# Kernel tuning notes

Hardware: AMD Instinct MI355X
Metric: run time of the kernel (lower is better)

The kernel has to match this reference:

```python
import jax, jax.numpy as jnp
import numpy as np

H = 512          # hidden_dim
T = 20           # output_seq_len
EPS = 1e-5


def _ln(x, g, b):
    m = jnp.mean(x, axis=-1, keepdims=True)
    v = jnp.mean((x - m) ** 2, axis=-1, keepdims=True)
    return (x - m) * jax.lax.rsqrt(v + EPS) * g + b


def setup_inputs() -> dict:
    key = jax.random.key(0)
    ks = jax.random.split(key, 20)
    N, LD, PD = 65536, 128, 32
    s = 0.02
    return {
        "z_q": jax.random.normal(ks[0], (N, LD), jnp.float32),
        "f_prior": jax.random.normal(ks[1], (N, PD), jnp.float32),
        # init_mlp: Linear(160 -> 1024) -> LN -> GELU -> Linear(1024 -> 512) -> Tanh
        "W1": jax.random.normal(ks[2], (LD + PD, 2 * H), jnp.float32) * s,
        "b1": jnp.zeros((2 * H,), jnp.float32),
        "g1": jnp.ones((2 * H,), jnp.float32),
        "be1": jnp.zeros((2 * H,), jnp.float32),
        "W2": jax.random.normal(ks[3], (2 * H, H), jnp.float32) * s,
        "b2": jnp.zeros((H,), jnp.float32),
        # start token (output_dim = 1)
        "start_token": jax.random.normal(ks[4], (1,), jnp.float32) * 0.1,
        # GRU, input_size=1, hidden_size=H, gates stacked [r, z, n] (torch layout)
        "W_ih": jax.random.normal(ks[5], (3 * H, 1), jnp.float32) * s,
        "W_hh": jax.random.normal(ks[6], (3 * H, H), jnp.float32) * s,
        "b_ih": jnp.zeros((3 * H,), jnp.float32),
        "b_hh": jnp.zeros((3 * H,), jnp.float32),
        # output_mlp: Linear(H -> H//2) -> LN -> GELU -> Linear(H//2 -> 1)
        "Wo1": jax.random.normal(ks[7], (H, H // 2), jnp.float32) * s,
        "bo1": jnp.zeros((H // 2,), jnp.float32),
        "go": jnp.ones((H // 2,), jnp.float32),
        "beo": jnp.zeros((H // 2,), jnp.float32),
        "Wo2": jax.random.normal(ks[8], (H // 2, 1), jnp.float32) * s,
        "bo2": jnp.zeros((1,), jnp.float32),
    }


def reference(z_q, f_prior, W1, b1, g1, be1, W2, b2, start_token,
              W_ih, W_hh, b_ih, b_hh, Wo1, bo1, go, beo, Wo2, bo2):
    N = z_q.shape[0]
    # init_mlp -> h_0 (dropout is identity at eval)
    combined = jnp.concatenate([z_q, f_prior], axis=1)          # (N, LD+PD)
    h = jnp.tanh(jax.nn.gelu(_ln(combined @ W1 + b1, g1, be1), approximate=False) @ W2 + b2)  # (N, H)

    x0 = jnp.broadcast_to(start_token[None, :], (N, 1))          # (N, 1)

    def step(carry, _):
        h, x = carry
        gi = x @ W_ih.T + b_ih                                   # (N, 3H)
        gh = h @ W_hh.T + b_hh                                   # (N, 3H)
        r = jax.nn.sigmoid(gi[:, :H] + gh[:, :H])
        z = jax.nn.sigmoid(gi[:, H:2 * H] + gh[:, H:2 * H])
        n = jnp.tanh(gi[:, 2 * H:] + r * gh[:, 2 * H:])
        h_new = (1.0 - z) * n + z * h
        y = jax.nn.gelu(_ln(h_new @ Wo1 + bo1, go, beo), approximate=False) @ Wo2 + bo2  # (N, 1)
        return (h_new, y), y

    _, ys = jax.lax.scan(step, (h, x0), None, length=T)          # (T, N, 1)
    preds = jnp.transpose(ys[..., 0], (1, 0))                    # (N, T), output_dim==1 squeeze
    return preds
```

## Files before the change

kernel.cpp:

```cpp
#include <hip/hip_runtime.h>
#include <math.h>


typedef _Float16 f16;
typedef _Float16 f16x4 __attribute__((ext_vector_type(4)));
typedef _Float16 f16x8 __attribute__((ext_vector_type(8)));
typedef float f32x4 __attribute__((ext_vector_type(4)));

#define TSTEPS 20

__device__ __forceinline__ float sigm(float v) { return 1.0f / (1.0f + __expf(-v)); }
__device__ __forceinline__ float tanh_s(float v) {
  float e = __expf(-2.0f * fabsf(v));
  float r = (1.0f - e) / (1.0f + e);
  return copysignf(r, v);
}
__device__ __forceinline__ float gelu_e(float v) {
  return 0.5f * v * (1.0f + erff(v * 0.70710678118654752f));
}
__device__ __forceinline__ void st4(float* d, float4 v) {
  d[0] = v.x; d[1] = v.y; d[2] = v.z; d[3] = v.w;
}

__device__ __forceinline__ int fa(int m, int k) {
  return (((k >> 5) * 4 + (m >> 4)) << 10) + (((m & 15) + ((k >> 3) & 3) * 16) << 4) + ((k & 7) * 2);
}

__global__ void cvt_weights(const float* __restrict__ W1, const float* __restrict__ W2,
                            const float* __restrict__ Whh, const float* __restrict__ Wo1,
                            const float* __restrict__ bih, const float* __restrict__ bhh,
                            f16* __restrict__ w1t, f16* __restrict__ w2t,
                            f16* __restrict__ whh, f16* __restrict__ wo1t,
                            float* __restrict__ bcr, float* __restrict__ bcz) {
  int i = blockIdx.x * 256 + threadIdx.x;
  if (i < 163840) { int n = i / 160; int k = i - n * 160; w1t[i] = (f16)W1[k * 1024 + n]; return; }
  i -= 163840;
  if (i < 524288) { int n = i >> 10; int k = i & 1023; w2t[i] = (f16)W2[k * 512 + n]; return; }
  i -= 524288;
  if (i < 786432) { whh[i] = (f16)Whh[i]; return; }
  i -= 786432;
  if (i < 131072) { int o = i >> 9; int k = i & 511; wo1t[i] = (f16)Wo1[k * 256 + o]; return; }
  i -= 131072;
  if (i < 512) { bcr[i] = bih[i] + bhh[i]; return; }
  i -= 512;
  if (i < 512) { bcz[i] = bih[512 + i] + bhh[512 + i]; return; }
}

__global__ __launch_bounds__(512, 2)
void gru_main(
    const float* __restrict__ zq, const float* __restrict__ fpr,
    const float* __restrict__ b1, const float* __restrict__ g1, const float* __restrict__ be1,
    const float* __restrict__ b2, const float* __restrict__ stok,
    const float* __restrict__ Wih, const float* __restrict__ bih, const float* __restrict__ bhh,
    const float* __restrict__ bo1, const float* __restrict__ go, const float* __restrict__ beo,
    const float* __restrict__ Wo2, const float* __restrict__ bo2,
    const f16* __restrict__ w1t, const f16* __restrict__ w2t,
    const f16* __restrict__ whh, const f16* __restrict__ wo1t,
    const float* __restrict__ bcr, const float* __restrict__ bcz,
    float* __restrict__ out) {
  __shared__ __align__(16) unsigned char sm[131072];
  __shared__ float sm_s[256], sm_ss[256], sm_yp[256];
  __shared__ float sm_x[64];

  const int tid = threadIdx.x;
  const int w = tid >> 6;
  const int lane = tid & 63;
  const int l16 = lane & 15;
  const int l4 = lane >> 4;
  const int R0 = blockIdx.x * 64;

  const float bo2v = bo2[0];
  if (tid < 64) sm_x[tid] = stok[0];

  #pragma unroll 1
  for (int p = 0; p < 4; ++p) {
    #pragma unroll 1
    for (int jh = 0; jh < 2; ++jh) {
      const int jq0 = w * 128 + p * 32 + jh * 16;
      f32x4 acc[4];
      #pragma unroll
      for (int mt = 0; mt < 4; ++mt) acc[mt] = (f32x4){0.f, 0.f, 0.f, 0.f};
      #pragma unroll
      for (int kf = 0; kf < 5; ++kf) {
        const int k0 = kf * 32 + l4 * 8;
        f16x8 B[4];
        #pragma unroll
        for (int mt = 0; mt < 4; ++mt) {
          const int gm = R0 + mt * 16 + l16;
          const float* src = (kf < 4) ? (zq + gm * 128 + k0) : (fpr + gm * 32 + (k0 - 128));
          float4 v0 = *(const float4*)src;
          float4 v1 = *(const float4*)(src + 4);
          f16x8 b;
          b[0] = (f16)v0.x; b[1] = (f16)v0.y; b[2] = (f16)v0.z; b[3] = (f16)v0.w;
          b[4] = (f16)v1.x; b[5] = (f16)v1.y; b[6] = (f16)v1.z; b[7] = (f16)v1.w;
          B[mt] = b;
        }
        const f16x8 A = *(const f16x8*)(w1t + (jq0 + l16) * 160 + k0);
        #pragma unroll
        for (int mt = 0; mt < 4; ++mt)
          acc[mt] = __builtin_amdgcn_mfma_f32_16x16x32_f16(A, B[mt], acc[mt], 0, 0, 0);
      }
      const int jq = jq0 + l4 * 4;
      float bb[4]; st4(bb, *(const float4*)(b1 + jq));
      #pragma unroll
      for (int mt = 0; mt < 4; ++mt) {
        f16x4 v;
        #pragma unroll
        for (int r = 0; r < 4; ++r) v[r] = (f16)(acc[mt][r] + bb[r]);
        *(f16x4*)(sm + fa(mt * 16 + l16, jq)) = v;
      }
    }
  }
  __syncthreads();
  {
    const int mt = w & 3, half = w >> 2;
    const int row = mt * 16 + l16;
    float s = 0.f, ss = 0.f;
    #pragma unroll 4
    for (int it = 0; it < 16; ++it) {
      const int kb = half * 16 + it;
      f16x8 v = *(const f16x8*)(sm + (kb * 4 + mt) * 1024 + lane * 16);
      #pragma unroll
      for (int i = 0; i < 8; ++i) { float f = (float)v[i]; s += f; ss += f * f; }
    }
    s += __shfl_xor(s, 16); ss += __shfl_xor(ss, 16);
    s += __shfl_xor(s, 32); ss += __shfl_xor(ss, 32);
    if (l4 == 0) { sm_s[row * 2 + half] = s; sm_ss[row * 2 + half] = ss; }
    __syncthreads();
    const float mean = (sm_s[row * 2] + sm_s[row * 2 + 1]) * (1.f / 1024.f);
    const float q2 = (sm_ss[row * 2] + sm_ss[row * 2 + 1]) * (1.f / 1024.f);
    const float rstd = rsqrtf(q2 - mean * mean + 1e-5f);
    #pragma unroll 2
    for (int it = 0; it < 16; ++it) {
      const int kb = half * 16 + it;
      const int off = (kb * 4 + mt) * 1024 + lane * 16;
      const int c = kb * 32 + l4 * 8;
      f16x8 v = *(const f16x8*)(sm + off);
      float4 ga = *(const float4*)(g1 + c);
      float4 gb = *(const float4*)(g1 + c + 4);
      float4 ba = *(const float4*)(be1 + c);
      float4 bb = *(const float4*)(be1 + c + 4);
      float gs[8] = {ga.x, ga.y, ga.z, ga.w, gb.x, gb.y, gb.z, gb.w};
      float bs[8] = {ba.x, ba.y, ba.z, ba.w, bb.x, bb.y, bb.z, bb.w};
      f16x8 o;
      #pragma unroll
      for (int i = 0; i < 8; ++i)
        o[i] = (f16)gelu_e(((float)v[i] - mean) * rstd * gs[i] + bs[i]);
      *(f16x8*)(sm + off) = o;
    }
  }
  __syncthreads();
  f16x4 hold[4][4];
  #pragma unroll 1
  for (int pp = 0; pp < 4; ++pp) {
    const int jq0 = w * 64 + pp * 16;
    f32x4 acc[4];
    #pragma unroll
    for (int mt = 0; mt < 4; ++mt) acc[mt] = (f32x4){0.f, 0.f, 0.f, 0.f};
    #pragma unroll 2
    for (int kf = 0; kf < 32; ++kf) {
      f16x8 B[4];
      #pragma unroll
      for (int mt = 0; mt < 4; ++mt)
        B[mt] = *(const f16x8*)(sm + (kf * 4 + mt) * 1024 + lane * 16);
      const f16x8 A = *(const f16x8*)(w2t + (jq0 + l16) * 1024 + kf * 32 + l4 * 8);
      #pragma unroll
      for (int mt = 0; mt < 4; ++mt)
        acc[mt] = __builtin_amdgcn_mfma_f32_16x16x32_f16(A, B[mt], acc[mt], 0, 0, 0);
    }
    const int jq = jq0 + l4 * 4;
    float bb[4]; st4(bb, *(const float4*)(b2 + jq));
    #pragma unroll
    for (int mt = 0; mt < 4; ++mt) {
      f16x4 v;
      #pragma unroll
      for (int r = 0; r < 4; ++r) v[r] = (f16)tanh_s(acc[mt][r] + bb[r]);
      hold[pp][mt] = v;
    }
  }
  __syncthreads();
  #pragma unroll
  for (int pp = 0; pp < 4; ++pp) {
    const int jq = w * 64 + pp * 16 + l4 * 4;
    #pragma unroll
    for (int mt = 0; mt < 4; ++mt)
      *(f16x4*)(sm + fa(mt * 16 + l16, jq)) = hold[pp][mt];
  }
  __syncthreads();

  #pragma unroll 1
  for (int t = 0; t < TSTEPS; ++t) {
    const int cur = (t & 1) << 16;
    const int nxt = cur ^ 65536;
    #pragma unroll 1
    for (int p = 0; p < 2; ++p) {
      f32x4 acc[4][3][2];
      #pragma unroll
      for (int mt = 0; mt < 4; ++mt)
        #pragma unroll
        for (int g = 0; g < 3; ++g)
          #pragma unroll
          for (int jh = 0; jh < 2; ++jh) acc[mt][g][jh] = (f32x4){0.f, 0.f, 0.f, 0.f};
      #pragma unroll 2
      for (int kf = 0; kf < 16; ++kf) {
        f16x8 B[4];
        #pragma unroll
        for (int mt = 0; mt < 4; ++mt)
          B[mt] = *(const f16x8*)(sm + cur + (kf * 4 + mt) * 1024 + lane * 16);
        #pragma unroll
        for (int g = 0; g < 3; ++g)
          #pragma unroll
          for (int jh = 0; jh < 2; ++jh) {
            const f16x8 A = *(const f16x8*)(whh + (g * 512 + w * 64 + p * 32 + jh * 16 + l16) * 512 + kf * 32 + l4 * 8);
            #pragma unroll
            for (int mt = 0; mt < 4; ++mt)
              acc[mt][g][jh] = __builtin_amdgcn_mfma_f32_16x16x32_f16(A, B[mt], acc[mt][g][jh], 0, 0, 0);
          }
      }
      if (p == 0) __syncthreads();
      #pragma unroll
      for (int jh = 0; jh < 2; ++jh) {
        const int jq = w * 64 + p * 32 + jh * 16 + l4 * 4;
        float wr[4], wz[4], wn[4], cr[4], cz[4], bn[4], cn[4];
        st4(wr, *(const float4*)(Wih + jq));
        st4(wz, *(const float4*)(Wih + 512 + jq));
        st4(wn, *(const float4*)(Wih + 1024 + jq));
        st4(cr, *(const float4*)(bcr + jq));
        st4(cz, *(const float4*)(bcz + jq));
        st4(bn, *(const float4*)(bih + 1024 + jq));
        st4(cn, *(const float4*)(bhh + 1024 + jq));
        #pragma unroll
        for (int mt = 0; mt < 4; ++mt) {
          const int m = mt * 16 + l16;
          const float x = sm_x[m];
          const int hoff = fa(m, jq);
          const f16x4 ho = *(const f16x4*)(sm + cur + hoff);
          f16x4 hn;
          #pragma unroll
          for (int r = 0; r < 4; ++r) {
            const float gr = sigm(x * wr[r] + cr[r] + acc[mt][0][jh][r]);
            const float gz = sigm(x * wz[r] + cz[r] + acc[mt][1][jh][r]);
            const float gn = tanh_s(x * wn[r] + bn[r] + gr * (acc[mt][2][jh][r] + cn[r]));
            hn[r] = (f16)((1.f - gz) * gn + gz * (float)ho[r]);
          }
          *(f16x4*)(sm + nxt + hoff) = hn;
        }
      }
    }
    __syncthreads();
    {
      const int mg = w >> 2, jg = w & 3;
      f32x4 a2[2][4];
      #pragma unroll
      for (int mi = 0; mi < 2; ++mi)
        #pragma unroll
        for (int jt2 = 0; jt2 < 4; ++jt2) a2[mi][jt2] = (f32x4){0.f, 0.f, 0.f, 0.f};
      #pragma unroll 2
      for (int kf = 0; kf < 16; ++kf) {
        f16x8 B[2];
        #pragma unroll
        for (int mi = 0; mi < 2; ++mi)
          B[mi] = *(const f16x8*)(sm + nxt + (kf * 4 + mg * 2 + mi) * 1024 + lane * 16);
        #pragma unroll
        for (int jt2 = 0; jt2 < 4; ++jt2) {
          const f16x8 A = *(const f16x8*)(wo1t + (jg * 64 + jt2 * 16 + l16) * 512 + kf * 32 + l4 * 8);
          #pragma unroll
          for (int mi = 0; mi < 2; ++mi)
            a2[mi][jt2] = __builtin_amdgcn_mfma_f32_16x16x32_f16(A, B[mi], a2[mi][jt2], 0, 0, 0);
        }
      }
      float vv[2][4][4];
      float bo1v[4][4];
      #pragma unroll
      for (int jt2 = 0; jt2 < 4; ++jt2)
        st4(bo1v[jt2], *(const float4*)(bo1 + jg * 64 + jt2 * 16 + l4 * 4));
      #pragma unroll
      for (int mi = 0; mi < 2; ++mi) {
        float s = 0.f, ss = 0.f;
        #pragma unroll
        for (int jt2 = 0; jt2 < 4; ++jt2)
          #pragma unroll
          for (int r = 0; r < 4; ++r) {
            const float v = a2[mi][jt2][r] + bo1v[jt2][r];
            vv[mi][jt2][r] = v; s += v; ss += v * v;
          }
        s += __shfl_xor(s, 16); ss += __shfl_xor(ss, 16);
        s += __shfl_xor(s, 32); ss += __shfl_xor(ss, 32);
        if (l4 == 0) {
          const int m = (mg * 2 + mi) * 16 + l16;
          sm_s[m * 4 + jg] = s;
          sm_ss[m * 4 + jg] = ss;
        }
      }
      __syncthreads();
      float gov[4][4], bev[4][4], wv[4][4];
      #pragma unroll
      for (int jt2 = 0; jt2 < 4; ++jt2) {
        const int jb = jg * 64 + jt2 * 16 + l4 * 4;
        st4(gov[jt2], *(const float4*)(go + jb));
        st4(bev[jt2], *(const float4*)(beo + jb));
        st4(wv[jt2], *(const float4*)(Wo2 + jb));
      }
      #pragma unroll
      for (int mi = 0; mi < 2; ++mi) {
        const int m = (mg * 2 + mi) * 16 + l16;
        float4 ps = *(const float4*)(sm_s + m * 4);
        float4 pq = *(const float4*)(sm_ss + m * 4);
        const float mean = (ps.x + ps.y + ps.z + ps.w) * (1.f / 256.f);
        const float q2 = (pq.x + pq.y + pq.z + pq.w) * (1.f / 256.f);
        const float rstd = rsqrtf(q2 - mean * mean + 1e-5f);
        float y = 0.f;
        #pragma unroll
        for (int jt2 = 0; jt2 < 4; ++jt2)
          #pragma unroll
          for (int r = 0; r < 4; ++r)
            y += gelu_e((vv[mi][jt2][r] - mean) * rstd * gov[jt2][r] + bev[jt2][r]) * wv[jt2][r];
        y += __shfl_xor(y, 16);
        y += __shfl_xor(y, 32);
        if (l4 == 0) sm_yp[m * 4 + jg] = y;
      }
      __syncthreads();
      if (tid < 64) {
        float4 ps = *(const float4*)(sm_yp + tid * 4);
        const float y = bo2v + ps.x + ps.y + ps.z + ps.w;
        sm_x[tid] = y;
        out[(R0 + tid) * 20 + t] = y;
      }
    }
  }
}

extern "C" void kernel_launch(void* const* d_in, const int* in_sizes, int n_in,
                              void* d_out, int out_size, void* d_ws, size_t ws_size,
                              hipStream_t stream) {
  const float* zq   = (const float*)d_in[0];
  const float* fpr  = (const float*)d_in[1];
  const float* W1   = (const float*)d_in[2];
  const float* b1   = (const float*)d_in[3];
  const float* g1   = (const float*)d_in[4];
  const float* be1  = (const float*)d_in[5];
  const float* W2   = (const float*)d_in[6];
  const float* b2   = (const float*)d_in[7];
  const float* stok = (const float*)d_in[8];
  const float* Wih  = (const float*)d_in[9];
  const float* Whh  = (const float*)d_in[10];
  const float* bih  = (const float*)d_in[11];
  const float* bhh  = (const float*)d_in[12];
  const float* Wo1  = (const float*)d_in[13];
  const float* bo1  = (const float*)d_in[14];
  const float* go   = (const float*)d_in[15];
  const float* beo  = (const float*)d_in[16];
  const float* Wo2  = (const float*)d_in[17];
  const float* bo2  = (const float*)d_in[18];

  char* ws = (char*)d_ws;
  f16* w1t   = (f16*)(ws + 0);
  f16* w2t   = (f16*)(ws + 327680);
  f16* whh   = (f16*)(ws + 1376256);
  f16* wo1t  = (f16*)(ws + 2949120);
  float* bcr = (float*)(ws + 3211264);
  float* bcz = (float*)(ws + 3213312);

  cvt_weights<<<6276, 256, 0, stream>>>(W1, W2, Whh, Wo1, bih, bhh,
                                        w1t, w2t, whh, wo1t, bcr, bcz);

  const int N = in_sizes[0] / 128;
  gru_main<<<N / 64, 512, 0, stream>>>(zq, fpr, b1, g1, be1, b2, stok, Wih, bih, bhh,
                                       bo1, go, beo, Wo2, bo2, w1t, w2t, whh, wo1t,
                                       bcr, bcz, (float*)d_out);
}
```

Before: 5.997 ms.

## Warp-specialize GRU step and output MLP, pipelining output of previous step

Waves 0-3 now compute the recurrent GRU matmul and gate blend for step t, while waves 4-7 compute the output MLP for step t-1 from the same hidden-state buffer. Each output wave owns a 16-row tile with the full 256-wide reduction, so the layer-norm statistics no longer need cross-wave shared-memory reductions and extra barriers. Gate weights, combined biases and output LN constants are staged in LDS as f16. The trade-off is that the GRU matmul runs on only half the waves, lengthening the critical path. The f16 constants slightly reduce precision.

```diff
diff --git a/kernel.cpp b/kernel.cpp
--- a/kernel.cpp
+++ b/kernel.cpp
@@ -26,12 +26,59 @@
   return (((k >> 5) * 4 + (m >> 4)) << 10) + (((m & 15) + ((k >> 3) & 3) * 16) << 4) + ((k & 7) * 2);
 }
 
+#define G1_MFMA(ACC, JT)                                                        \
+  {                                                                             \
+    _Pragma("unroll 2")                                                         \
+    for (int kf = 0; kf < 16; ++kf) {                                           \
+      f16x8 Bf[4];                                                              \
+      _Pragma("unroll")                                                         \
+      for (int mt = 0; mt < 4; ++mt)                                            \
+        Bf[mt] = *(const f16x8*)(sm + cur + ((kf * 4 + mt) << 10) + lane * 16); \
+      _Pragma("unroll")                                                         \
+      for (int g = 0; g < 3; ++g) {                                             \
+        const f16x8 Af = *(const f16x8*)(whh + (g * 512 + (JT) + l16) * 512 + kf * 32 + l4 * 8); \
+        _Pragma("unroll")                                                       \
+        for (int mt = 0; mt < 4; ++mt)                                          \
+          ACC[mt][g] = __builtin_amdgcn_mfma_f32_16x16x32_f16(Af, Bf[mt], ACC[mt][g], 0, 0, 0); \
+      }                                                                         \
+    }                                                                           \
+  }
+
+#define G1_BLEND(ACC, JT)                                                       \
+  {                                                                             \
+    const int jq = (JT) + l4 * 4;                                               \
+    const f16x4 wrh = *(const f16x4*)(sm_c7 + jq);                              \
+    const f16x4 wzh = *(const f16x4*)(sm_c7 + 512 + jq);                        \
+    const f16x4 wnh = *(const f16x4*)(sm_c7 + 1024 + jq);                       \
+    const f16x4 crh = *(const f16x4*)(sm_c7 + 1536 + jq);                       \
+    const f16x4 czh = *(const f16x4*)(sm_c7 + 2048 + jq);                       \
+    const f16x4 bnh = *(const f16x4*)(sm_c7 + 2560 + jq);                       \
+    const f16x4 cnh = *(const f16x4*)(sm_c7 + 3072 + jq);                       \
+    _Pragma("unroll")                                                           \
+    for (int mt = 0; mt < 4; ++mt) {                                            \
+      const int m = mt * 16 + l16;                                              \
+      const float x = sm_x[m];                                                  \
+      const int hoff = fa(m, jq);                                               \
+      const f16x4 ho = *(const f16x4*)(sm + cur + hoff);                        \
+      f16x4 hn;                                                                 \
+      _Pragma("unroll")                                                         \
+      for (int r = 0; r < 4; ++r) {                                             \
+        const float gr = sigm(x * (float)wrh[r] + (float)crh[r] + ACC[mt][0][r]); \
+        const float gz = sigm(x * (float)wzh[r] + (float)czh[r] + ACC[mt][1][r]); \
+        const float gn = tanh_s(x * (float)wnh[r] + (float)bnh[r] + gr * (ACC[mt][2][r] + (float)cnh[r])); \
+        hn[r] = (f16)((1.f - gz) * gn + gz * (float)ho[r]);                     \
+      }                                                                         \
+      *(f16x4*)(sm + nxt + hoff) = hn;                                          \
+    }                                                                           \
+  }
+
 __global__ void cvt_weights(const float* __restrict__ W1, const float* __restrict__ W2,
                             const float* __restrict__ Whh, const float* __restrict__ Wo1,
-                            const float* __restrict__ bih, const float* __restrict__ bhh,
+                            const float* __restrict__ Wih, const float* __restrict__ bih,
+                            const float* __restrict__ bhh,
                             f16* __restrict__ w1t, f16* __restrict__ w2t,
                             f16* __restrict__ whh, f16* __restrict__ wo1t,
-                            float* __restrict__ bcr, float* __restrict__ bcz) {
+                            f16* __restrict__ c7) {
   int i = blockIdx.x * 256 + threadIdx.x;
   if (i < 163840) { int n = i / 160; int k = i - n * 160; w1t[i] = (f16)W1[k * 1024 + n]; return; }
   i -= 163840;
@@ -41,9 +88,18 @@
   i -= 786432;
   if (i < 131072) { int o = i >> 9; int k = i & 511; wo1t[i] = (f16)Wo1[k * 256 + o]; return; }
   i -= 131072;
-  if (i < 512) { bcr[i] = bih[i] + bhh[i]; return; }
-  i -= 512;
-  if (i < 512) { bcz[i] = bih[512 + i] + bhh[512 + i]; return; }
+  if (i < 3584) {
+    const int which = i >> 9, j = i & 511;
+    float v;
+    if (which == 0) v = Wih[j];
+    else if (which == 1) v = Wih[512 + j];
+    else if (which == 2) v = Wih[1024 + j];
+    else if (which == 3) v = bih[j] + bhh[j];
+    else if (which == 4) v = bih[512 + j] + bhh[512 + j];
+    else if (which == 5) v = bih[1024 + j];
+    else v = bhh[1024 + j];
+    c7[i] = (f16)v;
+  }
 }
 
 __global__ __launch_bounds__(512, 2)
@@ -51,16 +107,17 @@
     const float* __restrict__ zq, const float* __restrict__ fpr,
     const float* __restrict__ b1, const float* __restrict__ g1, const float* __restrict__ be1,
     const float* __restrict__ b2, const float* __restrict__ stok,
-    const float* __restrict__ Wih, const float* __restrict__ bih, const float* __restrict__ bhh,
     const float* __restrict__ bo1, const float* __restrict__ go, const float* __restrict__ beo,
     const float* __restrict__ Wo2, const float* __restrict__ bo2,
     const f16* __restrict__ w1t, const f16* __restrict__ w2t,
     const f16* __restrict__ whh, const f16* __restrict__ wo1t,
-    const float* __restrict__ bcr, const float* __restrict__ bcz,
+    const f16* __restrict__ c7,
     float* __restrict__ out) {
   __shared__ __align__(16) unsigned char sm[131072];
-  __shared__ float sm_s[256], sm_ss[256], sm_yp[256];
+  __shared__ float sm_s[256], sm_ss[256];
   __shared__ float sm_x[64];
+  __shared__ __align__(8) f16 sm_c7[3584];
+  __shared__ __align__(8) f16 sm_aux[1024];
 
   const int tid = threadIdx.x;
   const int w = tid >> 6;
@@ -71,6 +128,12 @@
 
   const float bo2v = bo2[0];
   if (tid < 64) sm_x[tid] = stok[0];
+  for (int i = tid; i < 1792; i += 512)
+    ((unsigned*)sm_c7)[i] = ((const unsigned*)c7)[i];
+  for (int i = tid; i < 1024; i += 512) {
+    const float v = (i < 256) ? bo1[i] : (i < 512) ? go[i - 256] : (i < 768) ? beo[i - 512] : Wo2[i - 768];
+    sm_aux[i] = (f16)v;
+  }
 
   #pragma unroll 1
   for (int p = 0; p < 4; ++p) {
@@ -144,14 +207,14 @@
       float bs[8] = {ba.x, ba.y, ba.z, ba.w, bb.x, bb.y, bb.z, bb.w};
       f16x8 o;
       #pragma unroll
-      for (int i = 0; i < 8; ++i)
-        o[i] = (f16)gelu_e(((float)v[i] - mean) * rstd * gs[i] + bs[i]);
+      for (int j = 0; j < 8; ++j)
+        o[j] = (f16)gelu_e(((float)v[j] - mean) * rstd * gs[j] + bs[j]);
       *(f16x8*)(sm + off) = o;
     }
   }
   __syncthreads();
   f16x4 hold[4][4];
-  #pragma unroll 1
+  #pragma unroll
   for (int pp = 0; pp < 4; ++pp) {
     const int jq0 = w * 64 + pp * 16;
     f32x4 acc[4];
@@ -162,7 +225,7 @@
       f16x8 B[4];
       #pragma unroll
       for (int mt = 0; mt < 4; ++mt)
-        B[mt] = *(const f16x8*)(sm + (kf * 4 + mt) * 1024 + lane * 16);
+        B[mt] = *(const f16x8*)(sm + ((kf * 4 + mt) << 10) + lane * 16);
       const f16x8 A = *(const f16x8*)(w2t + (jq0 + l16) * 1024 + kf * 32 + l4 * 8);
       #pragma unroll
       for (int mt = 0; mt < 4; ++mt)
@@ -189,144 +252,85 @@
   __syncthreads();
 
   #pragma unroll 1
-  for (int t = 0; t < TSTEPS; ++t) {
+  for (int t = 0; t <= TSTEPS; ++t) {
     const int cur = (t & 1) << 16;
     const int nxt = cur ^ 65536;
-    #pragma unroll 1
-    for (int p = 0; p < 2; ++p) {
-      f32x4 acc[4][3][2];
-      #pragma unroll
-      for (int mt = 0; mt < 4; ++mt)
-        #pragma unroll
-        for (int g = 0; g < 3; ++g)
-          #pragma unroll
-          for (int jh = 0; jh < 2; ++jh) acc[mt][g][jh] = (f32x4){0.f, 0.f, 0.f, 0.f};
-      #pragma unroll 2
-      for (int kf = 0; kf < 16; ++kf) {
-        f16x8 B[4];
+    const int jt0 = w * 128;
+    f32x4 acc0[4][3];
+    if (w < 4) {
+      if (t < TSTEPS) {
         #pragma unroll
         for (int mt = 0; mt < 4; ++mt)
-          B[mt] = *(const f16x8*)(sm + cur + (kf * 4 + mt) * 1024 + lane * 16);
-        #pragma unroll
-        for (int g = 0; g < 3; ++g)
-          #pragma unroll
-          for (int jh = 0; jh < 2; ++jh) {
-            const f16x8 A = *(const f16x8*)(whh + (g * 512 + w * 64 + p * 32 + jh * 16 + l16) * 512 + kf * 32 + l4 * 8);
-            #pragma unroll
-            for (int mt = 0; mt < 4; ++mt)
-              acc[mt][g][jh] = __builtin_amdgcn_mfma_f32_16x16x32_f16(A, B[mt], acc[mt][g][jh], 0, 0, 0);
+          #pragma unroll
+          for (int g = 0; g < 3; ++g) acc0[mt][g] = (f32x4){0.f, 0.f, 0.f, 0.f};
+        G1_MFMA(acc0, jt0)
+      }
+    } else {
+      if (t >= 1) {
+        const int b = w - 4;
+        f32x4 a2[16];
+        #pragma unroll
+        for (int jt = 0; jt < 16; ++jt) a2[jt] = (f32x4){0.f, 0.f, 0.f, 0.f};
+        #pragma unroll 1
+        for (int kf = 0; kf < 16; ++kf) {
+          const f16x8 B = *(const f16x8*)(sm + cur + ((kf * 4 + b) << 10) + lane * 16);
+          #pragma unroll
+          for (int jt = 0; jt < 16; ++jt) {
+            const f16x8 A = *(const f16x8*)(wo1t + (jt * 16 + l16) * 512 + kf * 32 + l4 * 8);
+            a2[jt] = __builtin_amdgcn_mfma_f32_16x16x32_f16(A, B, a2[jt], 0, 0, 0);
           }
-      }
-      if (p == 0) __syncthreads();
-      #pragma unroll
-      for (int jh = 0; jh < 2; ++jh) {
-        const int jq = w * 64 + p * 32 + jh * 16 + l4 * 4;
-        float wr[4], wz[4], wn[4], cr[4], cz[4], bn[4], cn[4];
-        st4(wr, *(const float4*)(Wih + jq));
-        st4(wz, *(const float4*)(Wih + 512 + jq));
-        st4(wn, *(const float4*)(Wih + 1024 + jq));
-        st4(cr, *(const float4*)(bcr + jq));
-        st4(cz, *(const float4*)(bcz + jq));
-        st4(bn, *(const float4*)(bih + 1024 + jq));
-        st4(cn, *(const float4*)(bhh + 1024 + jq));
-        #pragma unroll
-        for (int mt = 0; mt < 4; ++mt) {
-          const int m = mt * 16 + l16;
-          const float x = sm_x[m];
-          const int hoff = fa(m, jq);
-          const f16x4 ho = *(const f16x4*)(sm + cur + hoff);
-          f16x4 hn;
+        }
+        float s = 0.f, ss = 0.f;
+        #pragma unroll
+        for (int jt = 0; jt < 16; ++jt) {
+          const f16x4 bb = *(const f16x4*)(sm_aux + jt * 16 + l4 * 4);
           #pragma unroll
           for (int r = 0; r < 4; ++r) {
-            const float gr = sigm(x * wr[r] + cr[r] + acc[mt][0][jh][r]);
-            const float gz = sigm(x * wz[r] + cz[r] + acc[mt][1][jh][r]);
-            const float gn = tanh_s(x * wn[r] + bn[r] + gr * (acc[mt][2][jh][r] + cn[r]));
-            hn[r] = (f16)((1.f - gz) * gn + gz * (float)ho[r]);
+            const float v = a2[jt][r] + (float)bb[r];
+            a2[jt][r] = v; s += v; ss += v * v;
           }
-          *(f16x4*)(sm + nxt + hoff) = hn;
-        }
-      }
-    }
-    __syncthreads();
-    {
-      const int mg = w >> 2, jg = w & 3;
-      f32x4 a2[2][4];
-      #pragma unroll
-      for (int mi = 0; mi < 2; ++mi)
-        #pragma unroll
-        for (int jt2 = 0; jt2 < 4; ++jt2) a2[mi][jt2] = (f32x4){0.f, 0.f, 0.f, 0.f};
-      #pragma unroll 2
-      for (int kf = 0; kf < 16; ++kf) {
-        f16x8 B[2];
-        #pragma unroll
-        for (int mi = 0; mi < 2; ++mi)
-          B[mi] = *(const f16x8*)(sm + nxt + (kf * 4 + mg * 2 + mi) * 1024 + lane * 16);
-        #pragma unroll
-        for (int jt2 = 0; jt2 < 4; ++jt2) {
-          const f16x8 A = *(const f16x8*)(wo1t + (jg * 64 + jt2 * 16 + l16) * 512 + kf * 32 + l4 * 8);
-          #pragma unroll
-          for (int mi = 0; mi < 2; ++mi)
-            a2[mi][jt2] = __builtin_amdgcn_mfma_f32_16x16x32_f16(A, B[mi], a2[mi][jt2], 0, 0, 0);
-        }
-      }
-      float vv[2][4][4];
-      float bo1v[4][4];
-      #pragma unroll
-      for (int jt2 = 0; jt2 < 4; ++jt2)
-        st4(bo1v[jt2], *(const float4*)(bo1 + jg * 64 + jt2 * 16 + l4 * 4));
-      #pragma unroll
-      for (int mi = 0; mi < 2; ++mi) {
-        float s = 0.f, ss = 0.f;
-        #pragma unroll
-        for (int jt2 = 0; jt2 < 4; ++jt2)
-          #pragma unroll
-          for (int r = 0; r < 4; ++r) {
-            const float v = a2[mi][jt2][r] + bo1v[jt2][r];
-            vv[mi][jt2][r] = v; s += v; ss += v * v;
-          }
+        }
         s += __shfl_xor(s, 16); ss += __shfl_xor(ss, 16);
         s += __shfl_xor(s, 32); ss += __shfl_xor(ss, 32);
-        if (l4 == 0) {
-          const int m = (mg * 2 + mi) * 16 + l16;
-          sm_s[m * 4 + jg] = s;
-          sm_ss[m * 4 + jg] = ss;
-        }
-      }
-      __syncthreads();
-      float gov[4][4], bev[4][4], wv[4][4];
-      #pragma unroll
-      for (int jt2 = 0; jt2 < 4; ++jt2) {
-        const int jb = jg * 64 + jt2 * 16 + l4 * 4;
-        st4(gov[jt2], *(const float4*)(go + jb));
-        st4(bev[jt2], *(const float4*)(beo + jb));
-        st4(wv[jt2], *(const float4*)(Wo2 + jb));
-      }
-      #pragma unroll
-      for (int mi = 0; mi < 2; ++mi) {
-        const int m = (mg * 2 + mi) * 16 + l16;
-        float4 ps = *(const float4*)(sm_s + m * 4);
-        float4 pq = *(const float4*)(sm_ss + m * 4);
-        const float mean = (ps.x + ps.y + ps.z + ps.w) * (1.f / 256.f);
-        const float q2 = (pq.x + pq.y + pq.z + pq.w) * (1.f / 256.f);
-        const float rstd = rsqrtf(q2 - mean * mean + 1e-5f);
+        const float mean = s * (1.f / 256.f);
+        const float rstd = rsqrtf(ss * (1.f / 256.f) - mean * mean + 1e-5f);
         float y = 0.f;
         #pragma unroll
-        for (int jt2 = 0; jt2 < 4; ++jt2)
+        for (int jt = 0; jt < 16; ++jt) {
+          const int jb = jt * 16 + l4 * 4;
+          const f16x4 gov = *(const f16x4*)(sm_aux + 256 + jb);
+          const f16x4 bev = *(const f16x4*)(sm_aux + 512 + jb);
+          const f16x4 wv  = *(const f16x4*)(sm_aux + 768 + jb);
           #pragma unroll
           for (int r = 0; r < 4; ++r)
-            y += gelu_e((vv[mi][jt2][r] - mean) * rstd * gov[jt2][r] + bev[jt2][r]) * wv[jt2][r];
+            y += gelu_e((a2[jt][r] - mean) * rstd * (float)gov[r] + (float)bev[r]) * (float)wv[r];
+        }
         y += __shfl_xor(y, 16);
         y += __shfl_xor(y, 32);
-        if (l4 == 0) sm_yp[m * 4 + jg] = y;
-      }
-      __syncthreads();
-      if (tid < 64) {
-        float4 ps = *(const float4*)(sm_yp + tid * 4);
-        const float y = bo2v + ps.x + ps.y + ps.z + ps.w;
-        sm_x[tid] = y;
-        out[(R0 + tid) * 20 + t] = y;
-      }
-    }
+        if (l4 == 0) {
+          const int m = b * 16 + l16;
+          const float yy = y + bo2v;
+          sm_x[m] = yy;
+          out[(R0 + m) * 20 + (t - 1)] = yy;
+        }
+      }
+    }
+    __syncthreads();
+    if (w < 4 && t < TSTEPS) {
+      G1_BLEND(acc0, jt0)
+      #pragma unroll 1
+      for (int q = 1; q < 8; ++q) {
+        const int jt = jt0 + q * 16;
+        f32x4 acc[4][3];
+        #pragma unroll
+        for (int mt = 0; mt < 4; ++mt)
+          #pragma unroll
+          for (int g = 0; g < 3; ++g) acc[mt][g] = (f32x4){0.f, 0.f, 0.f, 0.f};
+        G1_MFMA(acc, jt)
+        G1_BLEND(acc, jt)
+      }
+    }
+    __syncthreads();
   }
 }
 
@@ -354,18 +358,17 @@
   const float* bo2  = (const float*)d_in[18];
 
   char* ws = (char*)d_ws;
-  f16* w1t   = (f16*)(ws + 0);
-  f16* w2t   = (f16*)(ws + 327680);
-  f16* whh   = (f16*)(ws + 1376256);
-  f16* wo1t  = (f16*)(ws + 2949120);
-  float* bcr = (float*)(ws + 3211264);
-  float* bcz = (float*)(ws + 3213312);
-
-  cvt_weights<<<6276, 256, 0, stream>>>(W1, W2, Whh, Wo1, bih, bhh,
-                                        w1t, w2t, whh, wo1t, bcr, bcz);
+  f16* w1t  = (f16*)(ws + 0);
+  f16* w2t  = (f16*)(ws + 327680);
+  f16* whh  = (f16*)(ws + 1376256);
+  f16* wo1t = (f16*)(ws + 2949120);
+  f16* c7   = (f16*)(ws + 3211264);
+
+  cvt_weights<<<6287, 256, 0, stream>>>(W1, W2, Whh, Wo1, Wih, bih, bhh,
+                                        w1t, w2t, whh, wo1t, c7);
 
   const int N = in_sizes[0] / 128;
-  gru_main<<<N / 64, 512, 0, stream>>>(zq, fpr, b1, g1, be1, b2, stok, Wih, bih, bhh,
-                                       bo1, go, beo, Wo2, bo2, w1t, w2t, whh, wo1t,
-                                       bcr, bcz, (float*)d_out);
-}
+  gru_main<<<N / 64, 512, 0, stream>>>(zq, fpr, b1, g1, be1, b2, stok,
+                                       bo1, go, beo, Wo2, bo2,
+                                       w1t, w2t, whh, wo1t, c7, (float*)d_out);
+}
```

New measurement: 9.016 ms. 50.3% more time.
